# Performance work log

Measured on AMD Instinct MI355X. Metric: run time of the kernel, lower is better.

## Reference

```python
import jax, jax.numpy as jnp
import numpy as np

N = 32768      # total nodes (512 graphs x 64 padded nodes)
E = 262144     # edges (avg degree 8)
F_IN = 74      # atom feature dim
D0 = 128       # dim_embedding
D1 = 256       # hidden feats
B = 512        # batch_size (graphs)
NPG = 64       # nodes per graph
EPS = 1e-5     # BatchNorm1d eps


def setup_inputs() -> dict:
    key = jax.random.key(0)
    ks = jax.random.split(key, 8)
    def rn(k, shape, s=0.05):
        return jax.random.normal(k, shape, jnp.float32) * s
    # init_transform weight [D0, F_IN]; padding=True zeroes the last row
    W_init = rn(ks[0], (D0, F_IN)).at[-1].set(0.0)
    return {
        "node_feats": jax.random.normal(ks[1], (N, F_IN), jnp.float32),
        "W_init": W_init,
        "gcn_w1": rn(ks[2], (D0, D1)), "gcn_b1": jnp.zeros((D1,), jnp.float32),
        "res_w1": rn(ks[3], (D1, D0)), "res_b1": jnp.zeros((D1,), jnp.float32),
        "bn_g1": jnp.ones((D1,), jnp.float32), "bn_b1": jnp.zeros((D1,), jnp.float32),
        "gcn_w2": rn(ks[4], (D1, D1)), "gcn_b2": jnp.zeros((D1,), jnp.float32),
        "bn_g2": jnp.ones((D1,), jnp.float32), "bn_b2": jnp.zeros((D1,), jnp.float32),
        "edge_src": jax.random.randint(ks[5], (E,), 0, N),
        "edge_dst": jax.random.randint(ks[6], (E,), 0, N),
    }


def _agg(x, src, dst):
    # DGL GraphConv norm='both': D_out^{-1/2} gather-scatter D_in^{-1/2}, degrees clamped to >= 1
    ones = jnp.ones((src.shape[0],), x.dtype)
    deg_out = jnp.clip(jax.ops.segment_sum(ones, src, num_segments=N), 1.0)
    deg_in = jnp.clip(jax.ops.segment_sum(ones, dst, num_segments=N), 1.0)
    xs = x * jax.lax.rsqrt(deg_out)[:, None]
    agg = jax.ops.segment_sum(xs[src], dst, num_segments=N)  # [N, d]
    return agg * jax.lax.rsqrt(deg_in)[:, None]


def _bn(x, g, b):
    # BatchNorm1d training-mode: batch stats over node axis, biased var
    m = x.mean(0)
    v = x.var(0)
    return (x - m) * jax.lax.rsqrt(v + EPS) * g + b


def reference(node_feats, W_init, gcn_w1, gcn_b1, res_w1, res_b1, bn_g1, bn_b1,
              gcn_w2, gcn_b2, bn_g2, bn_b2, edge_src, edge_dst):
    h = node_feats @ W_init.T  # [N, D0]
    # layer 1: residual Linear 128->256, GCN(aggregate then weight, since in<out), GELU, BN
    res = h @ res_w1.T + res_b1
    g = jax.nn.gelu(_agg(h, edge_src, edge_dst) @ gcn_w1 + gcn_b1, approximate=False)
    h = _bn(g + res, bn_g1, bn_b1)
    # layer 2: Identity residual
    g = jax.nn.gelu(_agg(h, edge_src, edge_dst) @ gcn_w2 + gcn_b2, approximate=False)
    h = _bn(g + h, bn_g2, bn_b2)
    return h.reshape(B, NPG, D1)
```

## Files before the change

kernel.cpp:

```cpp
#include <hip/hip_runtime.h>
#include <hip/hip_bf16.h>
#include <math.h>

#define N_NODES 32768
#define E_EDGES 262144
#define F_INF   74
#define D0      128
#define D1      256
#define BN_EPS  1e-5f
#define RBLK    1024

typedef float f32x4 __attribute__((ext_vector_type(4)));
typedef short s16x8 __attribute__((ext_vector_type(8)));

__device__ __forceinline__ float b2f(ushort h) { return __uint_as_float(((unsigned)h) << 16); }
__device__ __forceinline__ ushort f2b(float f) {
    unsigned u = __float_as_uint(f);
    return (ushort)((u + 0x7FFFu + ((u >> 16) & 1u)) >> 16);
}
__device__ __forceinline__ float gelu_exact(float x) {
    return 0.5f * x * (1.0f + erff(x * 0.70710678118654752440f));
}


__global__ void k_degrees(const int* __restrict__ src, const int* __restrict__ dst,
                          int* __restrict__ deg) {
    int e = blockIdx.x * 256 + threadIdx.x;
    if (e < E_EDGES) {
        atomicAdd(&deg[src[e]], 1);
        atomicAdd(&deg[N_NODES + dst[e]], 1);
    }
}

__global__ __launch_bounds__(1024) void k_scan(const int* __restrict__ deg,
                                               int* __restrict__ row_off,
                                               float* __restrict__ rsq_out,
                                               float* __restrict__ rsq_in,
                                               int* __restrict__ cursor) {
    __shared__ int part[1024];
    int t = threadIdx.x;
    int base = t * 32;
    int loc[32];
    int s = 0;
    #pragma unroll
    for (int i = 0; i < 32; i++) { loc[i] = s; s += deg[N_NODES + base + i]; }
    part[t] = s;
    #pragma unroll
    for (int i = 0; i < 32; i++) {
        int n = base + i;
        int d_o = deg[n];           if (d_o < 1) d_o = 1;
        int d_i = deg[N_NODES + n]; if (d_i < 1) d_i = 1;
        rsq_out[n] = 1.0f / sqrtf((float)d_o);
        rsq_in[n]  = 1.0f / sqrtf((float)d_i);
        cursor[n] = 0;
    }
    __syncthreads();
    for (int off = 1; off < 1024; off <<= 1) {
        int v = 0;
        if (t >= off) v = part[t - off];
        __syncthreads();
        if (t >= off) part[t] += v;
        __syncthreads();
    }
    int pre = (t == 0) ? 0 : part[t - 1];
    #pragma unroll
    for (int i = 0; i < 32; i++) row_off[base + i] = pre + loc[i];
    if (t == 1023) row_off[N_NODES] = part[1023];
}

__global__ void k_fill(const int* __restrict__ src, const int* __restrict__ dst,
                       const int* __restrict__ row_off, int* __restrict__ cursor,
                       int* __restrict__ csr_src) {
    int e = blockIdx.x * 256 + threadIdx.x;
    if (e < E_EDGES) {
        int d = dst[e];
        int slot = atomicAdd(&cursor[d], 1);
        csr_src[row_off[d] + slot] = src[e];
    }
}

__global__ void k_prep(const float* __restrict__ Wi, const float* __restrict__ w1,
                       const float* __restrict__ rw, const float* __restrict__ w2,
                       float* __restrict__ WT, ushort* __restrict__ WB1,
                       ushort* __restrict__ RWB, ushort* __restrict__ WB2) {
    int idx = blockIdx.x * 256 + threadIdx.x;
    {
        int n = idx >> 8, k = idx & 255;
        WB2[idx] = f2b(w2[k * D1 + n]);
    }
    if (idx < D1 * D0) {
        int n = idx >> 7, k = idx & 127;
        WB1[idx] = f2b(w1[k * D1 + n]);
        RWB[idx] = f2b(rw[idx]);
    }
    if (idx < F_INF * D0) {
        int f = idx / D0, c = idx % D0;
        WT[f * D0 + c] = Wi[c * F_INF + f];
    }
}


__global__ __launch_bounds__(256) void k_init_gemm(
    const float* __restrict__ nf, const float* __restrict__ WT,
    ushort* __restrict__ h0) {
    __shared__ float sNF[64 * 76];
    int nb = blockIdx.x * 64;
    int tid = threadIdx.x;
    for (int idx = tid; idx < 64 * F_INF; idx += 256) {
        int row = idx / F_INF, f = idx % F_INF;
        sNF[row * 76 + f] = nf[(size_t)nb * F_INF + idx];
    }
    __syncthreads();
    int tc = tid & 31;
    int tn = tid >> 5;
    int c0 = tc * 4;
    float acc[8][4];
    #pragma unroll
    for (int i = 0; i < 8; i++)
        #pragma unroll
        for (int j = 0; j < 4; j++) acc[i][j] = 0.f;
    for (int k = 0; k < F_INF; k++) {
        float4 w = *reinterpret_cast<const float4*>(&WT[k * D0 + c0]);
        #pragma unroll
        for (int i = 0; i < 8; i++) {
            float a = sNF[(tn * 8 + i) * 76 + k];
            acc[i][0] += a * w.x; acc[i][1] += a * w.y;
            acc[i][2] += a * w.z; acc[i][3] += a * w.w;
        }
    }
    #pragma unroll
    for (int i = 0; i < 8; i++) {
        ushort4 o;
        o.x = f2b(acc[i][0]); o.y = f2b(acc[i][1]);
        o.z = f2b(acc[i][2]); o.w = f2b(acc[i][3]);
        *reinterpret_cast<ushort4*>(&h0[(size_t)(nb + tn * 8 + i) * D0 + c0]) = o;
    }
}


__global__ __launch_bounds__(512) void k_layer1f(
    const ushort* __restrict__ h0B,
    const float* __restrict__ rsq_out, const float* __restrict__ rsq_in,
    const int* __restrict__ row_off, const int* __restrict__ csr_src,
    const ushort* __restrict__ WB1, const ushort* __restrict__ RWB,
    const float* __restrict__ b1, const float* __restrict__ rb,
    ushort* __restrict__ t1B, float* __restrict__ partials) {
    __shared__ ushort sA[32 * 128];
    int tid = threadIdx.x;
    int rbase = blockIdx.x * 32;
    {
        int nloc = tid >> 4;
        int node = rbase + nloc;
        int f = (tid & 15) * 8;
        int beg = row_off[node], end = row_off[node + 1];
        float a[8];
        #pragma unroll
        for (int j = 0; j < 8; j++) a[j] = 0.f;
        int e = beg;
        for (; e + 3 < end; e += 4) {
            int s0 = csr_src[e], s1 = csr_src[e + 1], s2 = csr_src[e + 2], s3 = csr_src[e + 3];
            float c0 = rsq_out[s0], c1 = rsq_out[s1], c2 = rsq_out[s2], c3 = rsq_out[s3];
            s16x8 v0 = *reinterpret_cast<const s16x8*>(&h0B[(size_t)s0 * D0 + f]);
            s16x8 v1 = *reinterpret_cast<const s16x8*>(&h0B[(size_t)s1 * D0 + f]);
            s16x8 v2 = *reinterpret_cast<const s16x8*>(&h0B[(size_t)s2 * D0 + f]);
            s16x8 v3 = *reinterpret_cast<const s16x8*>(&h0B[(size_t)s3 * D0 + f]);
            #pragma unroll
            for (int j = 0; j < 8; j++)
                a[j] += b2f((ushort)v0[j]) * c0 + b2f((ushort)v1[j]) * c1 +
                        b2f((ushort)v2[j]) * c2 + b2f((ushort)v3[j]) * c3;
        }
        for (; e < end; e++) {
            int s = csr_src[e];
            float sc = rsq_out[s];
            s16x8 v = *reinterpret_cast<const s16x8*>(&h0B[(size_t)s * D0 + f]);
            #pragma unroll
            for (int j = 0; j < 8; j++) a[j] += b2f((ushort)v[j]) * sc;
        }
        float si = rsq_in[node];
        s16x8 o;
        #pragma unroll
        for (int j = 0; j < 8; j++) o[j] = (short)f2b(a[j] * si);
        int boff = nloc * 256 + ((f * 2) ^ ((nloc & 15) << 4));
        *reinterpret_cast<s16x8*>(((char*)sA) + boff) = o;
    }
    __syncthreads();
    int w = tid >> 6, lane = tid & 63, m = lane & 15, g4 = lane >> 4;
    int cb = w * 32;
    s16x8 BG[2][4], BR[2][4];
    #pragma unroll
    for (int nt = 0; nt < 2; nt++)
        #pragma unroll
        for (int j = 0; j < 4; j++) {
            BG[nt][j] = *reinterpret_cast<const s16x8*>(&WB1[(size_t)(cb + nt * 16 + m) * D0 + j * 32 + g4 * 8]);
            BR[nt][j] = *reinterpret_cast<const s16x8*>(&RWB[(size_t)(cb + nt * 16 + m) * D0 + j * 32 + g4 * 8]);
        }
    float bg[2], brv[2];
    #pragma unroll
    for (int nt = 0; nt < 2; nt++) {
        bg[nt]  = b1[cb + nt * 16 + m];
        brv[nt] = rb[cb + nt * 16 + m];
    }
    float ps[2] = {0.f, 0.f}, pq[2] = {0.f, 0.f};
    #pragma unroll
    for (int rt = 0; rt < 2; rt++) {
        int row = rt * 16 + m;
        s16x8 aA[4], aH[4];
        #pragma unroll
        for (int j = 0; j < 4; j++) {
            int boff = row * 256 + (((j * 4 + g4) * 16) ^ ((row & 15) << 4));
            aA[j] = *reinterpret_cast<const s16x8*>(((const char*)sA) + boff);
            aH[j] = *reinterpret_cast<const s16x8*>(&h0B[(size_t)(rbase + row) * D0 + j * 32 + g4 * 8]);
        }
        f32x4 accG[2], accR[2];
        #pragma unroll
        for (int nt = 0; nt < 2; nt++) {
            accG[nt] = (f32x4){0.f, 0.f, 0.f, 0.f};
            accR[nt] = (f32x4){0.f, 0.f, 0.f, 0.f};
        }
        #pragma unroll
        for (int j = 0; j < 4; j++)
            #pragma unroll
            for (int nt = 0; nt < 2; nt++) {
                accG[nt] = __builtin_amdgcn_mfma_f32_16x16x32_bf16(aA[j], BG[nt][j], accG[nt], 0, 0, 0);
                accR[nt] = __builtin_amdgcn_mfma_f32_16x16x32_bf16(aH[j], BR[nt][j], accR[nt], 0, 0, 0);
            }
        #pragma unroll
        for (int nt = 0; nt < 2; nt++) {
            int col = cb + nt * 16 + m;
            #pragma unroll
            for (int r = 0; r < 4; r++) {
                int orow = rbase + rt * 16 + g4 * 4 + r;
                float v = gelu_exact(accG[nt][r] + bg[nt]) + accR[nt][r] + brv[nt];
                t1B[(size_t)orow * D1 + col] = f2b(v);
                ps[nt] += v; pq[nt] += v * v;
            }
        }
    }
    #pragma unroll
    for (int nt = 0; nt < 2; nt++) {
        float s = ps[nt], q = pq[nt];
        s += __shfl_xor(s, 16); s += __shfl_xor(s, 32);
        q += __shfl_xor(q, 16); q += __shfl_xor(q, 32);
        if (g4 == 0) {
            int col = cb + nt * 16 + m;
            partials[(size_t)col * RBLK + blockIdx.x] = s;
            partials[(size_t)(256 + col) * RBLK + blockIdx.x] = q;
        }
    }
}


__global__ __launch_bounds__(512) void k_layer2f(
    const ushort* __restrict__ t1B,
    const float* __restrict__ sc1, const float* __restrict__ sh1,
    const float* __restrict__ rsq_out, const float* __restrict__ rsq_in,
    const int* __restrict__ row_off, const int* __restrict__ csr_src,
    const ushort* __restrict__ WB2, const float* __restrict__ b2,
    ushort* __restrict__ t2B, float* __restrict__ partials) {
    __shared__ ushort sA[32 * 256];
    int tid = threadIdx.x;
    int rbase = blockIdx.x * 32;
    {
        int nloc = tid >> 4;
        int node = rbase + nloc;
        int f0 = (tid & 15) * 8;
        int beg = row_off[node], end = row_off[node + 1];
        float a0[8], a1[8];
        #pragma unroll
        for (int j = 0; j < 8; j++) { a0[j] = 0.f; a1[j] = 0.f; }
        float ssum = 0.f;
        int e = beg;
        for (; e + 1 < end; e += 2) {
            int s0 = csr_src[e], s1 = csr_src[e + 1];
            float c0 = rsq_out[s0], c1 = rsq_out[s1];
            s16x8 v00 = *reinterpret_cast<const s16x8*>(&t1B[(size_t)s0 * D1 + f0]);
            s16x8 v01 = *reinterpret_cast<const s16x8*>(&t1B[(size_t)s0 * D1 + f0 + 128]);
            s16x8 v10 = *reinterpret_cast<const s16x8*>(&t1B[(size_t)s1 * D1 + f0]);
            s16x8 v11 = *reinterpret_cast<const s16x8*>(&t1B[(size_t)s1 * D1 + f0 + 128]);
            ssum += c0 + c1;
            #pragma unroll
            for (int j = 0; j < 8; j++) {
                a0[j] += b2f((ushort)v00[j]) * c0 + b2f((ushort)v10[j]) * c1;
                a1[j] += b2f((ushort)v01[j]) * c0 + b2f((ushort)v11[j]) * c1;
            }
        }
        for (; e < end; e++) {
            int s = csr_src[e];
            float sc = rsq_out[s];
            s16x8 v0 = *reinterpret_cast<const s16x8*>(&t1B[(size_t)s * D1 + f0]);
            s16x8 v1 = *reinterpret_cast<const s16x8*>(&t1B[(size_t)s * D1 + f0 + 128]);
            ssum += sc;
            #pragma unroll
            for (int j = 0; j < 8; j++) {
                a0[j] += b2f((ushort)v0[j]) * sc;
                a1[j] += b2f((ushort)v1[j]) * sc;
            }
        }
        float si = rsq_in[node];
        s16x8 o0, o1;
        #pragma unroll
        for (int j = 0; j < 8; j++) {
            o0[j] = (short)f2b((sc1[f0 + j] * a0[j] + sh1[f0 + j] * ssum) * si);
            o1[j] = (short)f2b((sc1[f0 + 128 + j] * a1[j] + sh1[f0 + 128 + j] * ssum) * si);
        }
        int swz = (nloc & 15) << 4;
        int b0 = nloc * 512 + ((f0 * 2) ^ swz);
        int b1_ = nloc * 512 + (((f0 + 128) * 2) ^ swz);
        *reinterpret_cast<s16x8*>(((char*)sA) + b0) = o0;
        *reinterpret_cast<s16x8*>(((char*)sA) + b1_) = o1;
    }
    __syncthreads();
    int w = tid >> 6, lane = tid & 63, m = lane & 15, g4 = lane >> 4;
    int cb = w * 32;
    s16x8 BG[2][8];
    #pragma unroll
    for (int nt = 0; nt < 2; nt++)
        #pragma unroll
        for (int j = 0; j < 8; j++)
            BG[nt][j] = *reinterpret_cast<const s16x8*>(&WB2[(size_t)(cb + nt * 16 + m) * D1 + j * 32 + g4 * 8]);
    float bg[2], a1c[2], s1c[2];
    #pragma unroll
    for (int nt = 0; nt < 2; nt++) {
        int col = cb + nt * 16 + m;
        bg[nt] = b2[col]; a1c[nt] = sc1[col]; s1c[nt] = sh1[col];
    }
    float ps[2] = {0.f, 0.f}, pq[2] = {0.f, 0.f};
    #pragma unroll
    for (int rt = 0; rt < 2; rt++) {
        int row = rt * 16 + m;
        s16x8 aA[8];
        #pragma unroll
        for (int j = 0; j < 8; j++) {
            int boff = row * 512 + (((j * 4 + g4) * 16) ^ ((row & 15) << 4));
            aA[j] = *reinterpret_cast<const s16x8*>(((const char*)sA) + boff);
        }
        f32x4 acc[2];
        #pragma unroll
        for (int nt = 0; nt < 2; nt++) acc[nt] = (f32x4){0.f, 0.f, 0.f, 0.f};
        #pragma unroll
        for (int j = 0; j < 8; j++)
            #pragma unroll
            for (int nt = 0; nt < 2; nt++)
                acc[nt] = __builtin_amdgcn_mfma_f32_16x16x32_bf16(aA[j], BG[nt][j], acc[nt], 0, 0, 0);
        #pragma unroll
        for (int nt = 0; nt < 2; nt++) {
            int col = cb + nt * 16 + m;
            #pragma unroll
            for (int r = 0; r < 4; r++) {
                int orow = rbase + rt * 16 + g4 * 4 + r;
                float h1v = fmaf(b2f(t1B[(size_t)orow * D1 + col]), a1c[nt], s1c[nt]);
                float v = gelu_exact(acc[nt][r] + bg[nt]) + h1v;
                t2B[(size_t)orow * D1 + col] = f2b(v);
                ps[nt] += v; pq[nt] += v * v;
            }
        }
    }
    #pragma unroll
    for (int nt = 0; nt < 2; nt++) {
        float s = ps[nt], q = pq[nt];
        s += __shfl_xor(s, 16); s += __shfl_xor(s, 32);
        q += __shfl_xor(q, 16); q += __shfl_xor(q, 32);
        if (g4 == 0) {
            int col = cb + nt * 16 + m;
            partials[(size_t)col * RBLK + blockIdx.x] = s;
            partials[(size_t)(256 + col) * RBLK + blockIdx.x] = q;
        }
    }
}


__global__ __launch_bounds__(256) void k_reduce(
    const float* __restrict__ partials, const float* __restrict__ g,
    const float* __restrict__ b, float* __restrict__ sc, float* __restrict__ sh) {
    int c = blockIdx.x;
    int t = threadIdx.x;
    const float* ps = partials + (size_t)c * RBLK;
    const float* pq = partials + (size_t)(256 + c) * RBLK;
    float s = ps[t] + ps[t + 256] + ps[t + 512] + ps[t + 768];
    float q = pq[t] + pq[t + 256] + pq[t + 512] + pq[t + 768];
    __shared__ float Ls[256], Lq[256];
    Ls[t] = s; Lq[t] = q;
    __syncthreads();
    for (int o = 128; o > 0; o >>= 1) {
        if (t < o) { Ls[t] += Ls[t + o]; Lq[t] += Lq[t + o]; }
        __syncthreads();
    }
    if (t == 0) {
        float m = Ls[0] * (1.0f / (float)N_NODES);
        float var = Lq[0] * (1.0f / (float)N_NODES) - m * m;
        float a = g[c] / sqrtf(var + BN_EPS);
        sc[c] = a;
        sh[c] = b[c] - m * a;
    }
}


__global__ __launch_bounds__(256) void k_apply(
    const ushort* __restrict__ t2B, const float* __restrict__ sc,
    const float* __restrict__ sh, float* __restrict__ out) {
    int idx = blockIdx.x * 256 + threadIdx.x;
    size_t base = (size_t)idx * 8;
    int c = (int)(base & 255);
    s16x8 v = *reinterpret_cast<const s16x8*>(&t2B[base]);
    float4 o0, o1;
    o0.x = fmaf(b2f((ushort)v[0]), sc[c + 0], sh[c + 0]);
    o0.y = fmaf(b2f((ushort)v[1]), sc[c + 1], sh[c + 1]);
    o0.z = fmaf(b2f((ushort)v[2]), sc[c + 2], sh[c + 2]);
    o0.w = fmaf(b2f((ushort)v[3]), sc[c + 3], sh[c + 3]);
    o1.x = fmaf(b2f((ushort)v[4]), sc[c + 4], sh[c + 4]);
    o1.y = fmaf(b2f((ushort)v[5]), sc[c + 5], sh[c + 5]);
    o1.z = fmaf(b2f((ushort)v[6]), sc[c + 6], sh[c + 6]);
    o1.w = fmaf(b2f((ushort)v[7]), sc[c + 7], sh[c + 7]);
    *reinterpret_cast<float4*>(&out[base]) = o0;
    *reinterpret_cast<float4*>(&out[base + 4]) = o1;
}


static inline size_t align256(size_t x) { return (x + 255) & ~(size_t)255; }

extern "C" void kernel_launch(void* const* d_in, const int* in_sizes, int n_in,
                              void* d_out, int out_size, void* d_ws, size_t ws_size,
                              hipStream_t stream) {
    const float* node_feats = (const float*)d_in[0];
    const float* W_init     = (const float*)d_in[1];
    const float* gcn_w1     = (const float*)d_in[2];
    const float* gcn_b1     = (const float*)d_in[3];
    const float* res_w1     = (const float*)d_in[4];
    const float* res_b1     = (const float*)d_in[5];
    const float* bn_g1      = (const float*)d_in[6];
    const float* bn_b1      = (const float*)d_in[7];
    const float* gcn_w2     = (const float*)d_in[8];
    const float* gcn_b2     = (const float*)d_in[9];
    const float* bn_g2      = (const float*)d_in[10];
    const float* bn_b2      = (const float*)d_in[11];
    const int*   edge_src   = (const int*)d_in[12];
    const int*   edge_dst   = (const int*)d_in[13];
    float* out = (float*)d_out;

    char* p = (char*)d_ws;
    size_t off = 0;
    auto take = [&](size_t bytes) { void* r = p + off; off += align256(bytes); return r; };

    ushort* h0B   = (ushort*)take((size_t)N_NODES * D0 * 2);
    ushort* t1B   = (ushort*)take((size_t)N_NODES * D1 * 2);
    ushort* t2B   = (ushort*)take((size_t)N_NODES * D1 * 2);
    float*  WT    = (float*)take((size_t)F_INF * D0 * 4);
    ushort* WB1   = (ushort*)take((size_t)D1 * D0 * 2);
    ushort* RWB   = (ushort*)take((size_t)D1 * D0 * 2);
    ushort* WB2   = (ushort*)take((size_t)D1 * D1 * 2);
    float*  part1 = (float*)take((size_t)2 * 256 * RBLK * 4);
    float*  part2 = (float*)take((size_t)2 * 256 * RBLK * 4);
    float*  sc1   = (float*)take(256 * 4);
    float*  sh1   = (float*)take(256 * 4);
    float*  sc2   = (float*)take(256 * 4);
    float*  sh2   = (float*)take(256 * 4);
    float*  rsq_out = (float*)take((size_t)N_NODES * 4);
    float*  rsq_in  = (float*)take((size_t)N_NODES * 4);
    int*    degi    = (int*)take((size_t)2 * N_NODES * 4);
    int*    cursor  = (int*)take((size_t)N_NODES * 4);
    int*    row_off = (int*)take((size_t)(N_NODES + 2) * 4);
    int*    csr_src = (int*)take((size_t)E_EDGES * 4);

    hipMemsetAsync(degi, 0, (size_t)2 * N_NODES * 4, stream);

    k_degrees<<<(E_EDGES + 255) / 256, 256, 0, stream>>>(edge_src, edge_dst, degi);
    k_scan<<<1, 1024, 0, stream>>>(degi, row_off, rsq_out, rsq_in, cursor);
    k_fill<<<(E_EDGES + 255) / 256, 256, 0, stream>>>(edge_src, edge_dst, row_off, cursor, csr_src);

    k_prep<<<(D1 * D1) / 256, 256, 0, stream>>>(W_init, gcn_w1, res_w1, gcn_w2, WT, WB1, RWB, WB2);

    k_init_gemm<<<N_NODES / 64, 256, 0, stream>>>(node_feats, WT, h0B);

    k_layer1f<<<RBLK, 512, 0, stream>>>(h0B, rsq_out, rsq_in, row_off, csr_src,
                                        WB1, RWB, gcn_b1, res_b1, t1B, part1);
    k_reduce<<<256, 256, 0, stream>>>(part1, bn_g1, bn_b1, sc1, sh1);

    k_layer2f<<<RBLK, 512, 0, stream>>>(t1B, sc1, sh1, rsq_out, rsq_in, row_off, csr_src,
                                        WB2, gcn_b2, t2B, part2);
    k_reduce<<<256, 256, 0, stream>>>(part2, bn_g2, bn_b2, sc2, sh2);

    k_apply<<<(N_NODES * D1 / 8) / 256, 256, 0, stream>>>(t2B, sc2, sh2, out);
}
```

Measured before the change: 218.5 us.

## Use MFMA for input projection and halve row tiles in fused GCN layers

The scalar FP32 init GEMM is replaced by a bf16 MFMA kernel. A prep pass now converts node features and W_init to bf16, with K padded from 74 to 96. The fused layer kernels process 16 rows per block instead of 32, doubling the block count and the BN partial count (RBLK 2048). In each block, 32 threads per node gather narrower feature slices, and weight and residual loads are issued before the gather to overlap latency. In exchange, the extra bf16 conversion pass writes and reads a padded copy of the node features, each block reloads weight fragments for half as many rows, and bf16 input rounding adds precision loss.

```diff
diff --git a/kernel.cpp b/kernel.cpp
--- a/kernel.cpp
+++ b/kernel.cpp
@@ -5,13 +5,15 @@
 #define N_NODES 32768
 #define E_EDGES 262144
 #define F_INF   74
+#define KP      96
 #define D0      128
 #define D1      256
 #define BN_EPS  1e-5f
-#define RBLK    1024
+#define RBLK    2048
 
 typedef float f32x4 __attribute__((ext_vector_type(4)));
 typedef short s16x8 __attribute__((ext_vector_type(8)));
+typedef short s16x4 __attribute__((ext_vector_type(4)));
 
 __device__ __forceinline__ float b2f(ushort h) { return __uint_as_float(((unsigned)h) << 16); }
 __device__ __forceinline__ ushort f2b(float f) {
@@ -79,62 +81,55 @@
     }
 }
 
-__global__ void k_prep(const float* __restrict__ Wi, const float* __restrict__ w1,
-                       const float* __restrict__ rw, const float* __restrict__ w2,
-                       float* __restrict__ WT, ushort* __restrict__ WB1,
-                       ushort* __restrict__ RWB, ushort* __restrict__ WB2) {
+
+__global__ void k_prep(const float* __restrict__ nf, const float* __restrict__ Wi,
+                       const float* __restrict__ w1, const float* __restrict__ rw,
+                       const float* __restrict__ w2,
+                       ushort* __restrict__ nfB, ushort* __restrict__ WTB,
+                       ushort* __restrict__ WB1, ushort* __restrict__ RWB,
+                       ushort* __restrict__ WB2) {
     int idx = blockIdx.x * 256 + threadIdx.x;
     {
-        int n = idx >> 8, k = idx & 255;
-        WB2[idx] = f2b(w2[k * D1 + n]);
+        int n = idx / KP, k = idx - n * KP;
+        nfB[idx] = (k < F_INF) ? f2b(nf[n * F_INF + k]) : (ushort)0;
+    }
+    if (idx < D0 * KP) {
+        int c = idx / KP, k = idx - c * KP;
+        WTB[idx] = (k < F_INF) ? f2b(Wi[c * F_INF + k]) : (ushort)0;
     }
     if (idx < D1 * D0) {
         int n = idx >> 7, k = idx & 127;
         WB1[idx] = f2b(w1[k * D1 + n]);
         RWB[idx] = f2b(rw[idx]);
     }
-    if (idx < F_INF * D0) {
-        int f = idx / D0, c = idx % D0;
-        WT[f * D0 + c] = Wi[c * F_INF + f];
-    }
-}
-
-
-__global__ __launch_bounds__(256) void k_init_gemm(
-    const float* __restrict__ nf, const float* __restrict__ WT,
+    if (idx < D1 * D1) {
+        int n = idx >> 8, k = idx & 255;
+        WB2[idx] = f2b(w2[k * D1 + n]);
+    }
+}
+
+
+__global__ __launch_bounds__(512) void k_init_mfma(
+    const ushort* __restrict__ nfB, const ushort* __restrict__ WTB,
     ushort* __restrict__ h0) {
-    __shared__ float sNF[64 * 76];
-    int nb = blockIdx.x * 64;
     int tid = threadIdx.x;
-    for (int idx = tid; idx < 64 * F_INF; idx += 256) {
-        int row = idx / F_INF, f = idx % F_INF;
-        sNF[row * 76 + f] = nf[(size_t)nb * F_INF + idx];
-    }
-    __syncthreads();
-    int tc = tid & 31;
-    int tn = tid >> 5;
-    int c0 = tc * 4;
-    float acc[8][4];
-    #pragma unroll
-    for (int i = 0; i < 8; i++)
-        #pragma unroll
-        for (int j = 0; j < 4; j++) acc[i][j] = 0.f;
-    for (int k = 0; k < F_INF; k++) {
-        float4 w = *reinterpret_cast<const float4*>(&WT[k * D0 + c0]);
-        #pragma unroll
-        for (int i = 0; i < 8; i++) {
-            float a = sNF[(tn * 8 + i) * 76 + k];
-            acc[i][0] += a * w.x; acc[i][1] += a * w.y;
-            acc[i][2] += a * w.z; acc[i][3] += a * w.w;
-        }
-    }
-    #pragma unroll
-    for (int i = 0; i < 8; i++) {
-        ushort4 o;
-        o.x = f2b(acc[i][0]); o.y = f2b(acc[i][1]);
-        o.z = f2b(acc[i][2]); o.w = f2b(acc[i][3]);
-        *reinterpret_cast<ushort4*>(&h0[(size_t)(nb + tn * 8 + i) * D0 + c0]) = o;
-    }
+    int w = tid >> 6, lane = tid & 63, m = lane & 15, g4 = lane >> 4;
+    int col = w * 16 + m;
+    int rbase = blockIdx.x * 16;
+    s16x8 B[3], A[3];
+    #pragma unroll
+    for (int j = 0; j < 3; j++)
+        B[j] = *reinterpret_cast<const s16x8*>(&WTB[(size_t)col * KP + j * 32 + g4 * 8]);
+    #pragma unroll
+    for (int j = 0; j < 3; j++)
+        A[j] = *reinterpret_cast<const s16x8*>(&nfB[(size_t)(rbase + m) * KP + j * 32 + g4 * 8]);
+    f32x4 acc = (f32x4){0.f, 0.f, 0.f, 0.f};
+    #pragma unroll
+    for (int j = 0; j < 3; j++)
+        acc = __builtin_amdgcn_mfma_f32_16x16x32_bf16(A[j], B[j], acc, 0, 0, 0);
+    #pragma unroll
+    for (int r = 0; r < 4; r++)
+        h0[(size_t)(rbase + g4 * 4 + r) * D0 + col] = f2b(acc[r]);
 }
 
 
@@ -145,95 +140,93 @@
     const ushort* __restrict__ WB1, const ushort* __restrict__ RWB,
     const float* __restrict__ b1, const float* __restrict__ rb,
     ushort* __restrict__ t1B, float* __restrict__ partials) {
-    __shared__ ushort sA[32 * 128];
+    __shared__ ushort sA[16 * 128];
     int tid = threadIdx.x;
-    int rbase = blockIdx.x * 32;
+    int rbase = blockIdx.x * 16;
+    int w = tid >> 6, lane = tid & 63, m = lane & 15, g4 = lane >> 4;
+    int cb = w * 32;
+    s16x8 BG[2][4], BR[2][4], aH[4];
+    #pragma unroll
+    for (int nt = 0; nt < 2; nt++)
+        #pragma unroll
+        for (int j = 0; j < 4; j++) {
+            BG[nt][j] = *reinterpret_cast<const s16x8*>(&WB1[(size_t)(cb + nt * 16 + m) * D0 + j * 32 + g4 * 8]);
+            BR[nt][j] = *reinterpret_cast<const s16x8*>(&RWB[(size_t)(cb + nt * 16 + m) * D0 + j * 32 + g4 * 8]);
+        }
+    #pragma unroll
+    for (int j = 0; j < 4; j++)
+        aH[j] = *reinterpret_cast<const s16x8*>(&h0B[(size_t)(rbase + m) * D0 + j * 32 + g4 * 8]);
+    float bg[2], brv[2];
+    #pragma unroll
+    for (int nt = 0; nt < 2; nt++) {
+        bg[nt]  = b1[cb + nt * 16 + m];
+        brv[nt] = rb[cb + nt * 16 + m];
+    }
     {
-        int nloc = tid >> 4;
+        int nloc = tid >> 5;
         int node = rbase + nloc;
-        int f = (tid & 15) * 8;
+        int f = (tid & 31) * 4;
         int beg = row_off[node], end = row_off[node + 1];
-        float a[8];
-        #pragma unroll
-        for (int j = 0; j < 8; j++) a[j] = 0.f;
+        float a[4];
+        #pragma unroll
+        for (int j = 0; j < 4; j++) a[j] = 0.f;
         int e = beg;
         for (; e + 3 < end; e += 4) {
             int s0 = csr_src[e], s1 = csr_src[e + 1], s2 = csr_src[e + 2], s3 = csr_src[e + 3];
             float c0 = rsq_out[s0], c1 = rsq_out[s1], c2 = rsq_out[s2], c3 = rsq_out[s3];
-            s16x8 v0 = *reinterpret_cast<const s16x8*>(&h0B[(size_t)s0 * D0 + f]);
-            s16x8 v1 = *reinterpret_cast<const s16x8*>(&h0B[(size_t)s1 * D0 + f]);
-            s16x8 v2 = *reinterpret_cast<const s16x8*>(&h0B[(size_t)s2 * D0 + f]);
-            s16x8 v3 = *reinterpret_cast<const s16x8*>(&h0B[(size_t)s3 * D0 + f]);
+            s16x4 v0 = *reinterpret_cast<const s16x4*>(&h0B[(size_t)s0 * D0 + f]);
+            s16x4 v1 = *reinterpret_cast<const s16x4*>(&h0B[(size_t)s1 * D0 + f]);
+            s16x4 v2 = *reinterpret_cast<const s16x4*>(&h0B[(size_t)s2 * D0 + f]);
+            s16x4 v3 = *reinterpret_cast<const s16x4*>(&h0B[(size_t)s3 * D0 + f]);
             #pragma unroll
-            for (int j = 0; j < 8; j++)
+            for (int j = 0; j < 4; j++)
                 a[j] += b2f((ushort)v0[j]) * c0 + b2f((ushort)v1[j]) * c1 +
                         b2f((ushort)v2[j]) * c2 + b2f((ushort)v3[j]) * c3;
         }
         for (; e < end; e++) {
             int s = csr_src[e];
             float sc = rsq_out[s];
-            s16x8 v = *reinterpret_cast<const s16x8*>(&h0B[(size_t)s * D0 + f]);
+            s16x4 v = *reinterpret_cast<const s16x4*>(&h0B[(size_t)s * D0 + f]);
             #pragma unroll
-            for (int j = 0; j < 8; j++) a[j] += b2f((ushort)v[j]) * sc;
+            for (int j = 0; j < 4; j++) a[j] += b2f((ushort)v[j]) * sc;
         }
         float si = rsq_in[node];
-        s16x8 o;
-        #pragma unroll
-        for (int j = 0; j < 8; j++) o[j] = (short)f2b(a[j] * si);
-        int boff = nloc * 256 + ((f * 2) ^ ((nloc & 15) << 4));
-        *reinterpret_cast<s16x8*>(((char*)sA) + boff) = o;
+        s16x4 o;
+        #pragma unroll
+        for (int j = 0; j < 4; j++) o[j] = (short)f2b(a[j] * si);
+        int boff = nloc * 256 + (((tid & 31) * 8) ^ ((nloc & 15) << 4));
+        *reinterpret_cast<s16x4*>(((char*)sA) + boff) = o;
     }
     __syncthreads();
-    int w = tid >> 6, lane = tid & 63, m = lane & 15, g4 = lane >> 4;
-    int cb = w * 32;
-    s16x8 BG[2][4], BR[2][4];
-    #pragma unroll
-    for (int nt = 0; nt < 2; nt++)
-        #pragma unroll
-        for (int j = 0; j < 4; j++) {
-            BG[nt][j] = *reinterpret_cast<const s16x8*>(&WB1[(size_t)(cb + nt * 16 + m) * D0 + j * 32 + g4 * 8]);
-            BR[nt][j] = *reinterpret_cast<const s16x8*>(&RWB[(size_t)(cb + nt * 16 + m) * D0 + j * 32 + g4 * 8]);
-        }
-    float bg[2], brv[2];
-    #pragma unroll
-    for (int nt = 0; nt < 2; nt++) {
-        bg[nt]  = b1[cb + nt * 16 + m];
-        brv[nt] = rb[cb + nt * 16 + m];
-    }
+    s16x8 aA[4];
+    #pragma unroll
+    for (int j = 0; j < 4; j++) {
+        int boff = m * 256 + ((((j * 4 + g4) * 16)) ^ ((m & 15) << 4));
+        aA[j] = *reinterpret_cast<const s16x8*>(((const char*)sA) + boff);
+    }
+    f32x4 accG[2], accR[2];
+    #pragma unroll
+    for (int nt = 0; nt < 2; nt++) {
+        accG[nt] = (f32x4){0.f, 0.f, 0.f, 0.f};
+        accR[nt] = (f32x4){0.f, 0.f, 0.f, 0.f};
+    }
+    #pragma unroll
+    for (int j = 0; j < 4; j++)
+        #pragma unroll
+        for (int nt = 0; nt < 2; nt++) {
+            accG[nt] = __builtin_amdgcn_mfma_f32_16x16x32_bf16(aA[j], BG[nt][j], accG[nt], 0, 0, 0);
+            accR[nt] = __builtin_amdgcn_mfma_f32_16x16x32_bf16(aH[j], BR[nt][j], accR[nt], 0, 0, 0);
+        }
     float ps[2] = {0.f, 0.f}, pq[2] = {0.f, 0.f};
     #pragma unroll
-    for (int rt = 0; rt < 2; rt++) {
-        int row = rt * 16 + m;
-        s16x8 aA[4], aH[4];
-        #pragma unroll
-        for (int j = 0; j < 4; j++) {
-            int boff = row * 256 + (((j * 4 + g4) * 16) ^ ((row & 15) << 4));
-            aA[j] = *reinterpret_cast<const s16x8*>(((const char*)sA) + boff);
-            aH[j] = *reinterpret_cast<const s16x8*>(&h0B[(size_t)(rbase + row) * D0 + j * 32 + g4 * 8]);
-        }
-        f32x4 accG[2], accR[2];
-        #pragma unroll
-        for (int nt = 0; nt < 2; nt++) {
-            accG[nt] = (f32x4){0.f, 0.f, 0.f, 0.f};
-            accR[nt] = (f32x4){0.f, 0.f, 0.f, 0.f};
-        }
-        #pragma unroll
-        for (int j = 0; j < 4; j++)
-            #pragma unroll
-            for (int nt = 0; nt < 2; nt++) {
-                accG[nt] = __builtin_amdgcn_mfma_f32_16x16x32_bf16(aA[j], BG[nt][j], accG[nt], 0, 0, 0);
-                accR[nt] = __builtin_amdgcn_mfma_f32_16x16x32_bf16(aH[j], BR[nt][j], accR[nt], 0, 0, 0);
-            }
-        #pragma unroll
-        for (int nt = 0; nt < 2; nt++) {
-            int col = cb + nt * 16 + m;
-            #pragma unroll
-            for (int r = 0; r < 4; r++) {
-                int orow = rbase + rt * 16 + g4 * 4 + r;
-                float v = gelu_exact(accG[nt][r] + bg[nt]) + accR[nt][r] + brv[nt];
-                t1B[(size_t)orow * D1 + col] = f2b(v);
-                ps[nt] += v; pq[nt] += v * v;
-            }
+    for (int nt = 0; nt < 2; nt++) {
+        int col = cb + nt * 16 + m;
+        #pragma unroll
+        for (int r = 0; r < 4; r++) {
+            int orow = rbase + g4 * 4 + r;
+            float v = gelu_exact(accG[nt][r] + bg[nt]) + accR[nt][r] + brv[nt];
+            t1B[(size_t)orow * D1 + col] = f2b(v);
+            ps[nt] += v; pq[nt] += v * v;
         }
     }
     #pragma unroll
@@ -257,102 +250,92 @@
     const int* __restrict__ row_off, const int* __restrict__ csr_src,
     const ushort* __restrict__ WB2, const float* __restrict__ b2,
     ushort* __restrict__ t2B, float* __restrict__ partials) {
-    __shared__ ushort sA[32 * 256];
+    __shared__ ushort sA[16 * 256];
     int tid = threadIdx.x;
-    int rbase = blockIdx.x * 32;
+    int rbase = blockIdx.x * 16;
+    int w = tid >> 6, lane = tid & 63, m = lane & 15, g4 = lane >> 4;
+    int cb = w * 32;
+    s16x8 BG[2][8];
+    #pragma unroll
+    for (int nt = 0; nt < 2; nt++)
+        #pragma unroll
+        for (int j = 0; j < 8; j++)
+            BG[nt][j] = *reinterpret_cast<const s16x8*>(&WB2[(size_t)(cb + nt * 16 + m) * D1 + j * 32 + g4 * 8]);
+    float bg[2], a1c[2], s1c[2];
+    ushort rres[2][4];
+    #pragma unroll
+    for (int nt = 0; nt < 2; nt++) {
+        int col = cb + nt * 16 + m;
+        bg[nt] = b2[col]; a1c[nt] = sc1[col]; s1c[nt] = sh1[col];
+        #pragma unroll
+        for (int r = 0; r < 4; r++)
+            rres[nt][r] = t1B[(size_t)(rbase + g4 * 4 + r) * D1 + col];
+    }
     {
-        int nloc = tid >> 4;
+        int nloc = tid >> 5;
         int node = rbase + nloc;
-        int f0 = (tid & 15) * 8;
+        int f = (tid & 31) * 8;
         int beg = row_off[node], end = row_off[node + 1];
-        float a0[8], a1[8];
-        #pragma unroll
-        for (int j = 0; j < 8; j++) { a0[j] = 0.f; a1[j] = 0.f; }
+        float a[8];
+        #pragma unroll
+        for (int j = 0; j < 8; j++) a[j] = 0.f;
         float ssum = 0.f;
         int e = beg;
-        for (; e + 1 < end; e += 2) {
-            int s0 = csr_src[e], s1 = csr_src[e + 1];
-            float c0 = rsq_out[s0], c1 = rsq_out[s1];
-            s16x8 v00 = *reinterpret_cast<const s16x8*>(&t1B[(size_t)s0 * D1 + f0]);
-            s16x8 v01 = *reinterpret_cast<const s16x8*>(&t1B[(size_t)s0 * D1 + f0 + 128]);
-            s16x8 v10 = *reinterpret_cast<const s16x8*>(&t1B[(size_t)s1 * D1 + f0]);
-            s16x8 v11 = *reinterpret_cast<const s16x8*>(&t1B[(size_t)s1 * D1 + f0 + 128]);
-            ssum += c0 + c1;
+        for (; e + 3 < end; e += 4) {
+            int s0 = csr_src[e], s1 = csr_src[e + 1], s2 = csr_src[e + 2], s3 = csr_src[e + 3];
+            float c0 = rsq_out[s0], c1 = rsq_out[s1], c2 = rsq_out[s2], c3 = rsq_out[s3];
+            s16x8 v0 = *reinterpret_cast<const s16x8*>(&t1B[(size_t)s0 * D1 + f]);
+            s16x8 v1 = *reinterpret_cast<const s16x8*>(&t1B[(size_t)s1 * D1 + f]);
+            s16x8 v2 = *reinterpret_cast<const s16x8*>(&t1B[(size_t)s2 * D1 + f]);
+            s16x8 v3 = *reinterpret_cast<const s16x8*>(&t1B[(size_t)s3 * D1 + f]);
+            ssum += c0 + c1 + c2 + c3;
             #pragma unroll
-            for (int j = 0; j < 8; j++) {
-                a0[j] += b2f((ushort)v00[j]) * c0 + b2f((ushort)v10[j]) * c1;
-                a1[j] += b2f((ushort)v01[j]) * c0 + b2f((ushort)v11[j]) * c1;
-            }
+            for (int j = 0; j < 8; j++)
+                a[j] += b2f((ushort)v0[j]) * c0 + b2f((ushort)v1[j]) * c1 +
+                        b2f((ushort)v2[j]) * c2 + b2f((ushort)v3[j]) * c3;
         }
         for (; e < end; e++) {
             int s = csr_src[e];
             float sc = rsq_out[s];
-            s16x8 v0 = *reinterpret_cast<const s16x8*>(&t1B[(size_t)s * D1 + f0]);
-            s16x8 v1 = *reinterpret_cast<const s16x8*>(&t1B[(size_t)s * D1 + f0 + 128]);
+            s16x8 v = *reinterpret_cast<const s16x8*>(&t1B[(size_t)s * D1 + f]);
             ssum += sc;
             #pragma unroll
-            for (int j = 0; j < 8; j++) {
-                a0[j] += b2f((ushort)v0[j]) * sc;
-                a1[j] += b2f((ushort)v1[j]) * sc;
-            }
+            for (int j = 0; j < 8; j++) a[j] += b2f((ushort)v[j]) * sc;
         }
         float si = rsq_in[node];
-        s16x8 o0, o1;
-        #pragma unroll
-        for (int j = 0; j < 8; j++) {
-            o0[j] = (short)f2b((sc1[f0 + j] * a0[j] + sh1[f0 + j] * ssum) * si);
-            o1[j] = (short)f2b((sc1[f0 + 128 + j] * a1[j] + sh1[f0 + 128 + j] * ssum) * si);
-        }
-        int swz = (nloc & 15) << 4;
-        int b0 = nloc * 512 + ((f0 * 2) ^ swz);
-        int b1_ = nloc * 512 + (((f0 + 128) * 2) ^ swz);
-        *reinterpret_cast<s16x8*>(((char*)sA) + b0) = o0;
-        *reinterpret_cast<s16x8*>(((char*)sA) + b1_) = o1;
+        s16x8 o;
+        #pragma unroll
+        for (int j = 0; j < 8; j++)
+            o[j] = (short)f2b((sc1[f + j] * a[j] + sh1[f + j] * ssum) * si);
+        int boff = nloc * 512 + (((tid & 31) * 16) ^ ((nloc & 15) << 4));
+        *reinterpret_cast<s16x8*>(((char*)sA) + boff) = o;
     }
     __syncthreads();
-    int w = tid >> 6, lane = tid & 63, m = lane & 15, g4 = lane >> 4;
-    int cb = w * 32;
-    s16x8 BG[2][8];
-    #pragma unroll
-    for (int nt = 0; nt < 2; nt++)
-        #pragma unroll
-        for (int j = 0; j < 8; j++)
-            BG[nt][j] = *reinterpret_cast<const s16x8*>(&WB2[(size_t)(cb + nt * 16 + m) * D1 + j * 32 + g4 * 8]);
-    float bg[2], a1c[2], s1c[2];
+    s16x8 aA[8];
+    #pragma unroll
+    for (int j = 0; j < 8; j++) {
+        int boff = m * 512 + (((j * 4 + g4) * 16) ^ ((m & 15) << 4));
+        aA[j] = *reinterpret_cast<const s16x8*>(((const char*)sA) + boff);
+    }
+    f32x4 acc[2];
+    #pragma unroll
+    for (int nt = 0; nt < 2; nt++) acc[nt] = (f32x4){0.f, 0.f, 0.f, 0.f};
+    #pragma unroll
+    for (int j = 0; j < 8; j++)
+        #pragma unroll
+        for (int nt = 0; nt < 2; nt++)
+            acc[nt] = __builtin_amdgcn_mfma_f32_16x16x32_bf16(aA[j], BG[nt][j], acc[nt], 0, 0, 0);
+    float ps[2] = {0.f, 0.f}, pq[2] = {0.f, 0.f};
     #pragma unroll
     for (int nt = 0; nt < 2; nt++) {
         int col = cb + nt * 16 + m;
-        bg[nt] = b2[col]; a1c[nt] = sc1[col]; s1c[nt] = sh1[col];
-    }
-    float ps[2] = {0.f, 0.f}, pq[2] = {0.f, 0.f};
-    #pragma unroll
-    for (int rt = 0; rt < 2; rt++) {
-        int row = rt * 16 + m;
-        s16x8 aA[8];
-        #pragma unroll
-        for (int j = 0; j < 8; j++) {
-            int boff = row * 512 + (((j * 4 + g4) * 16) ^ ((row & 15) << 4));
-            aA[j] = *reinterpret_cast<const s16x8*>(((const char*)sA) + boff);
-        }
-        f32x4 acc[2];
-        #pragma unroll
-        for (int nt = 0; nt < 2; nt++) acc[nt] = (f32x4){0.f, 0.f, 0.f, 0.f};
-        #pragma unroll
-        for (int j = 0; j < 8; j++)
-            #pragma unroll
-            for (int nt = 0; nt < 2; nt++)
-                acc[nt] = __builtin_amdgcn_mfma_f32_16x16x32_bf16(aA[j], BG[nt][j], acc[nt], 0, 0, 0);
-        #pragma unroll
-        for (int nt = 0; nt < 2; nt++) {
-            int col = cb + nt * 16 + m;
-            #pragma unroll
-            for (int r = 0; r < 4; r++) {
-                int orow = rbase + rt * 16 + g4 * 4 + r;
-                float h1v = fmaf(b2f(t1B[(size_t)orow * D1 + col]), a1c[nt], s1c[nt]);
-                float v = gelu_exact(acc[nt][r] + bg[nt]) + h1v;
-                t2B[(size_t)orow * D1 + col] = f2b(v);
-                ps[nt] += v; pq[nt] += v * v;
-            }
+        #pragma unroll
+        for (int r = 0; r < 4; r++) {
+            int orow = rbase + g4 * 4 + r;
+            float h1v = fmaf(b2f(rres[nt][r]), a1c[nt], s1c[nt]);
+            float v = gelu_exact(acc[nt][r] + bg[nt]) + h1v;
+            t2B[(size_t)orow * D1 + col] = f2b(v);
+            ps[nt] += v; pq[nt] += v * v;
         }
     }
     #pragma unroll
@@ -376,8 +359,9 @@
     int t = threadIdx.x;
     const float* ps = partials + (size_t)c * RBLK;
     const float* pq = partials + (size_t)(256 + c) * RBLK;
-    float s = ps[t] + ps[t + 256] + ps[t + 512] + ps[t + 768];
-    float q = pq[t] + pq[t + 256] + pq[t + 512] + pq[t + 768];
+    float s = 0.f, q = 0.f;
+    #pragma unroll
+    for (int k = 0; k < 8; k++) { s += ps[t + 256 * k]; q += pq[t + 256 * k]; }
     __shared__ float Ls[256], Lq[256];
     Ls[t] = s; Lq[t] = q;
     __syncthreads();
@@ -444,7 +428,8 @@
     ushort* h0B   = (ushort*)take((size_t)N_NODES * D0 * 2);
     ushort* t1B   = (ushort*)take((size_t)N_NODES * D1 * 2);
     ushort* t2B   = (ushort*)take((size_t)N_NODES * D1 * 2);
-    float*  WT    = (float*)take((size_t)F_INF * D0 * 4);
+    ushort* nfB   = (ushort*)take((size_t)N_NODES * KP * 2);
+    ushort* WTB   = (ushort*)take((size_t)D0 * KP * 2);
     ushort* WB1   = (ushort*)take((size_t)D1 * D0 * 2);
     ushort* RWB   = (ushort*)take((size_t)D1 * D0 * 2);
     ushort* WB2   = (ushort*)take((size_t)D1 * D1 * 2);
@@ -467,9 +452,10 @@
     k_scan<<<1, 1024, 0, stream>>>(degi, row_off, rsq_out, rsq_in, cursor);
     k_fill<<<(E_EDGES + 255) / 256, 256, 0, stream>>>(edge_src, edge_dst, row_off, cursor, csr_src);
 
-    k_prep<<<(D1 * D1) / 256, 256, 0, stream>>>(W_init, gcn_w1, res_w1, gcn_w2, WT, WB1, RWB, WB2);
-
-    k_init_gemm<<<N_NODES / 64, 256, 0, stream>>>(node_feats, WT, h0B);
+    k_prep<<<(N_NODES * KP) / 256, 256, 0, stream>>>(node_feats, W_init, gcn_w1, res_w1, gcn_w2,
+                                                     nfB, WTB, WB1, RWB, WB2);
+
+    k_init_mfma<<<N_NODES / 16, 512, 0, stream>>>(nfB, WTB, h0B);
 
     k_layer1f<<<RBLK, 512, 0, stream>>>(h0B, rsq_out, rsq_in, row_off, csr_src,
                                         WB1, RWB, gcn_b1, res_b1, t1B, part1);
```

After: 256.9 us. +17.5%, slower.
